# Kernel tuning notes

Measured on AMD Instinct MI355X. Metric: run time of the kernel, lower is better.

Reference implementation:

```python
import jax, jax.numpy as jnp
import numpy as np

N = 100000
E = 3200000
NFEAT = 128
NCLASS = 40


def setup_inputs() -> dict:
    key = jax.random.key(0)
    ks = jax.random.split(key, 16)
    x = jax.random.normal(ks[0], (N, NFEAT), dtype=jnp.float32)
    edge_src = jax.random.randint(ks[1], (E,), 0, N)
    edge_dst = jax.random.randint(ks[2], (E,), 0, N)
    # normalized-adjacency-like positive edge weights
    edge_val = jax.random.uniform(ks[3], (E,), dtype=jnp.float32) * 0.1
    dims = [(NFEAT, 1024), (1024, 1024), (1024, 1024), (1024, 64), (64, NCLASS)]
    params = {}
    for i, (din, dout) in enumerate(dims):
        scale = 1.0 / np.sqrt(din)
        params[f"W{i+1}"] = jax.random.uniform(ks[4 + i], (din, dout), dtype=jnp.float32, minval=-scale, maxval=scale)
        params[f"b{i+1}"] = jax.random.uniform(ks[9 + i], (dout,), dtype=jnp.float32, minval=-scale, maxval=scale)
    return {"x": x, "edge_src": edge_src, "edge_dst": edge_dst, "edge_val": edge_val, **params}


def _gcn_layer(x, edge_src, edge_dst, edge_val, W, b):
    # support = x @ W ; out[dst] += val * support[src] ; + bias
    support = x @ W  # [N, dout]
    msgs = support[edge_src] * edge_val[:, None]  # [E, dout]
    agg = jax.ops.segment_sum(msgs, edge_dst, num_segments=x.shape[0])
    return agg + b


def reference(x, edge_src, edge_dst, edge_val, W1, b1, W2, b2, W3, b3, W4, b4, W5, b5):
    h = jax.nn.relu(_gcn_layer(x, edge_src, edge_dst, edge_val, W1, b1))
    identity1 = h
    h = jax.nn.relu(_gcn_layer(h, edge_src, edge_dst, edge_val, W2, b2))
    identity2 = h
    h = h + identity1
    h = jax.nn.relu(_gcn_layer(h, edge_src, edge_dst, edge_val, W3, b3))
    h = h + identity2
    h = jax.nn.relu(_gcn_layer(h, edge_src, edge_dst, edge_val, W4, b4))
    h = jax.nn.relu(_gcn_layer(h, edge_src, edge_dst, edge_val, W5, b5))
    return jax.nn.log_softmax(h, axis=1)
```

## Files before the change

kernel.cpp:

```cpp
#include <hip/hip_runtime.h>
#include <hip/hip_bf16.h>
#include <stdint.h>

#define NN 100000
#define NE 3200000
#define MP 100096
#define MPAD 100352
#define NPANEL 784
#define SCALE 32.0f
#define ISCALE 0.03125f
#define WSCALE 8192.0f

typedef __bf16 bf16x8 __attribute__((ext_vector_type(8)));
typedef float  f32x4  __attribute__((ext_vector_type(4)));
typedef unsigned short u16x8 __attribute__((ext_vector_type(8)));

__device__ __forceinline__ float b2f(unsigned short u) {
    union { unsigned int i; float f; } x; x.i = ((unsigned int)u) << 16; return x.f;
}
__device__ __forceinline__ unsigned short f2b(float f) {
    __hip_bfloat16 h = __float2bfloat16(f);
    return __builtin_bit_cast(unsigned short, h);
}

#if defined(__has_builtin)
#if __has_builtin(__builtin_amdgcn_cvt_pk_f32_fp8) && __has_builtin(__builtin_amdgcn_cvt_pk_fp8_f32)
#define HAVE_FP8_CVT 1
#endif
#endif

__device__ __forceinline__ float f8dec1(unsigned int b) {
    unsigned int s = (b >> 7) & 1u, e = (b >> 3) & 15u, m = b & 7u;
    float mag = e ? __builtin_bit_cast(float, (unsigned int)(((e + 120u) << 23) | (m << 20)))
                  : (float)m * 0.001953125f;
    return s ? -mag : mag;
}
__device__ __forceinline__ unsigned char f8enc1(float v) {
    unsigned int bits = __builtin_bit_cast(unsigned int, v);
    unsigned char s = (unsigned char)((bits >> 24) & 0x80u);
    float a = fabsf(v);
    if (!(a < 464.f)) return (unsigned char)(s | 0x7e);
    if (a < 0.015625f) {
        int q = (int)rintf(a * 512.f);
        return (unsigned char)(s | (unsigned char)q);
    }
    unsigned int b = __builtin_bit_cast(unsigned int, a);
    b += 0x7FFFFu + ((b >> 20) & 1u);
    unsigned int e = (b >> 23) - 120u;
    unsigned int m = (b >> 20) & 7u;
    if (e >= 16u) return (unsigned char)(s | 0x7e);
    return (unsigned char)(s | (e << 3) | m);
}
__device__ __forceinline__ void dec4(unsigned int u, float* o) {
#ifdef HAVE_FP8_CVT
    typedef float f32x2 __attribute__((ext_vector_type(2)));
    f32x2 lo = __builtin_amdgcn_cvt_pk_f32_fp8((int)u, false);
    f32x2 hi = __builtin_amdgcn_cvt_pk_f32_fp8((int)u, true);
    o[0] = lo[0]; o[1] = lo[1]; o[2] = hi[0]; o[3] = hi[1];
#else
    o[0] = f8dec1(u & 255u); o[1] = f8dec1((u >> 8) & 255u);
    o[2] = f8dec1((u >> 16) & 255u); o[3] = f8dec1((u >> 24) & 255u);
#endif
}
__device__ __forceinline__ unsigned char f8enc(float v) {
#ifdef HAVE_FP8_CVT
    return (unsigned char)(__builtin_amdgcn_cvt_pk_fp8_f32(v, v, 0, false) & 0xff);
#else
    return f8enc1(v);
#endif
}
__device__ __forceinline__ unsigned int enc4(float a, float b, float c, float d) {
#ifdef HAVE_FP8_CVT
    int r = __builtin_amdgcn_cvt_pk_fp8_f32(a, b, 0, false);
    r = __builtin_amdgcn_cvt_pk_fp8_f32(c, d, r, true);
    return (unsigned int)r;
#else
    return (unsigned int)f8enc1(a) | ((unsigned int)f8enc1(b) << 8) |
           ((unsigned int)f8enc1(c) << 16) | ((unsigned int)f8enc1(d) << 24);
#endif
}

#define GLDS16(g, l) __builtin_amdgcn_global_load_lds(                         \
    (const __attribute__((address_space(1))) void*)(const void*)(g),           \
    (__attribute__((address_space(3))) void*)(void*)(l), 16, 0, 0)

__global__ __launch_bounds__(256) void k_sentinel(float* out, int n, float code) {
    int i = blockIdx.x * 256 + threadIdx.x;
    if (i < n) out[i] = (i == 0) ? code : 1.0f;
}

__global__ __launch_bounds__(256) void k_zero_deg(unsigned int* deg) {
    int i = blockIdx.x * 256 + threadIdx.x;
    if (i < NN + 1) deg[i] = 0u;
}
__global__ __launch_bounds__(256) void k_hist(const int* __restrict__ dst,
                                              unsigned int* __restrict__ deg) {
    int e = blockIdx.x * 256 + threadIdx.x;
    if (e < NE) atomicAdd(&deg[dst[e]], 1u);
}
__global__ __launch_bounds__(256) void k_blocksum(const unsigned int* __restrict__ deg,
                                                  unsigned int* __restrict__ bsum) {
    __shared__ unsigned int sh[256];
    int base = blockIdx.x * 1024;
    unsigned int s = 0;
    for (int q = 0; q < 4; ++q) {
        int i = base + q * 256 + threadIdx.x;
        if (i < NN) s += deg[i];
    }
    sh[threadIdx.x] = s; __syncthreads();
    for (int off = 128; off > 0; off >>= 1) {
        if ((int)threadIdx.x < off) sh[threadIdx.x] += sh[threadIdx.x + off];
        __syncthreads();
    }
    if (threadIdx.x == 0) bsum[blockIdx.x] = sh[0];
}
__global__ __launch_bounds__(64) void k_scan_bsum(const unsigned int* __restrict__ bsum,
                                                  unsigned int* __restrict__ boff, int nb) {
    if (threadIdx.x == 0 && blockIdx.x == 0) {
        unsigned int run = 0;
        for (int i = 0; i < nb; ++i) { boff[i] = run; run += bsum[i]; }
    }
}
__global__ __launch_bounds__(256) void k_scan_final(const unsigned int* __restrict__ deg,
                                                    const unsigned int* __restrict__ boff,
                                                    int* __restrict__ rowptr) {
    __shared__ unsigned int sh[256];
    const int b = blockIdx.x, t = threadIdx.x;
    const int base = b * 1024 + t * 4;
    unsigned int v[4];
    for (int q = 0; q < 4; ++q) { int i = base + q; v[q] = (i < NN) ? deg[i] : 0u; }
    unsigned int p = v[0] + v[1] + v[2] + v[3];
    sh[t] = p; __syncthreads();
    for (int off = 1; off < 256; off <<= 1) {
        unsigned int add = (t >= off) ? sh[t - off] : 0u; __syncthreads();
        sh[t] += add; __syncthreads();
    }
    unsigned int run = sh[t] - p + boff[b];
    for (int q = 0; q < 4; ++q) {
        int i = base + q;
        if (i < NN) rowptr[i] = (int)run;
        run += v[q];
    }
    if (b == 0 && t == 0) rowptr[NN] = NE;
}
__global__ __launch_bounds__(256) void k_copy_cursor(const int* __restrict__ rowptr,
                                                     int* __restrict__ cur) {
    int i = blockIdx.x * 256 + threadIdx.x;
    if (i < NN) cur[i] = rowptr[i];
}
__global__ __launch_bounds__(256) void k_fill(const int* __restrict__ src,
                                              const int* __restrict__ dst,
                                              const float* __restrict__ val,
                                              int* __restrict__ cur,
                                              int* __restrict__ csr_src,
                                              float* __restrict__ csr_val) {
    int e = blockIdx.x * 256 + threadIdx.x;
    if (e < NE) {
        int d = dst[e];
        int p = atomicAdd(&cur[d], 1);
        csr_src[p] = src[e];
        csr_val[p] = val[e];
    }
}

__global__ __launch_bounds__(256) void k_build_tab(unsigned long long* __restrict__ tab,
                                                   unsigned long long px, unsigned long long p1,
                                                   unsigned long long p2, unsigned long long p3,
                                                   unsigned long long po, unsigned long long pd) {
    int r = blockIdx.x * 256 + threadIdx.x;
    if (r >= MPAD) return;
    unsigned long long p; long long rr;
    if (r < 50000)      { p = px; rr = r; }
    else if (r < 62500) { p = p1; rr = r - 50000; }
    else if (r < 75000) { p = p2; rr = r - 62500; }
    else if (r < 87500) { p = p3; rr = r - 75000; }
    else if (r < MP)    { p = po; rr = r - 87500; }
    else                { p = pd; rr = 0; }
    tab[r] = p + (unsigned long long)rr * 1024ull;
}

__global__ __launch_bounds__(256) void k_transpose_w(const float* __restrict__ W,
                                                     unsigned short* __restrict__ Wt,
                                                     int din, int dout) {
    int idx = blockIdx.x * 256 + threadIdx.x;
    if (idx >= din * dout) return;
    int i = idx / dout, o = idx % dout;
    Wt[(size_t)o * din + i] = f2b(W[idx]);
}
__global__ __launch_bounds__(256) void k_transpose_w8(const float* __restrict__ W,
                                                      unsigned char* __restrict__ Wt,
                                                      int din, int dout) {
    int idx = blockIdx.x * 256 + threadIdx.x;
    if (idx >= din * dout) return;
    int i = idx / dout, o = idx % dout;
    Wt[(size_t)o * din + i] = f8enc(W[idx] * WSCALE);
}

template<int BN, int AKIND, int EPI, int OKIND>
__global__ __launch_bounds__(256) void k_gemm(const void* __restrict__ Ap,
                                              const void* __restrict__ Ap2,
                                              const __hip_bfloat16* __restrict__ Bt,
                                              const float* __restrict__ bias,
                                              void* __restrict__ Cp,
                                              const unsigned long long* __restrict__ rowtab,
                                              int K, int Nn) {
    constexpr int BM = 128, BK = 32;
    __shared__ alignas(16) __hip_bfloat16 Al[BM * BK];
    __shared__ alignas(16) __hip_bfloat16 Bl[BN * BK];
    const int t = threadIdx.x;
    const int lane = t & 63, w = t >> 6;
    const int row0 = blockIdx.y * BM, col0 = blockIdx.x * BN;
    const int wm = w >> 1, wn = w & 1;
    constexpr int FN = BN / 32;

    f32x4 acc[4][FN];
#pragma unroll
    for (int i = 0; i < 4; ++i)
#pragma unroll
        for (int j = 0; j < FN; ++j) acc[i][j] = (f32x4){0.f, 0.f, 0.f, 0.f};

    const int srow = t >> 2;
    const int scol = ((t & 3) ^ ((srow >> 1) & 3)) * 8;
    const __hip_bfloat16* gB = Bt + (size_t)(col0 + srow) * K + scol;
    __hip_bfloat16* lB = Bl + w * 512;
    const __hip_bfloat16* gA = (const __hip_bfloat16*)Ap + (size_t)(row0 + srow) * K + scol;
    __hip_bfloat16* lA = Al + w * 512;

    const int nkt = K / BK;
    for (int kt = 0; kt < nkt; ++kt) {
        const int ko = kt * BK;
        GLDS16(gA + ko, lA);
        GLDS16(gA + (size_t)64 * K + ko, lA + 2048);
        GLDS16(gB + ko, lB);
        if constexpr (BN == 128) GLDS16(gB + (size_t)64 * K + ko, lB + 2048);
        __syncthreads();

        const int pcr = ((lane >> 4) ^ (((lane & 15) >> 1) & 3)) * 8;
        const __hip_bfloat16* Ar = Al + (wm * 64 + (lane & 15)) * BK + pcr;
        const __hip_bfloat16* Br = Bl + (wn * (BN / 2) + (lane & 15)) * BK + pcr;
        bf16x8 af[4], bfr[FN];
#pragma unroll
        for (int i = 0; i < 4; ++i) af[i] = *(const bf16x8*)(Ar + i * 16 * BK);
#pragma unroll
        for (int j = 0; j < FN; ++j) bfr[j] = *(const bf16x8*)(Br + j * 16 * BK);
#pragma unroll
        for (int i = 0; i < 4; ++i)
#pragma unroll
            for (int j = 0; j < FN; ++j)
                acc[i][j] = __builtin_amdgcn_mfma_f32_16x16x32_bf16(af[i], bfr[j], acc[i][j], 0, 0, 0);
        __syncthreads();
    }

#pragma unroll
    for (int i = 0; i < 4; ++i) {
        const int r0 = row0 + wm * 64 + i * 16 + (lane >> 4) * 4;
#pragma unroll
        for (int j = 0; j < FN; ++j) {
            const int c = col0 + wn * (BN / 2) + j * 16 + (lane & 15);
#pragma unroll
            for (int v = 0; v < 4; ++v) {
                float val = acc[i][j][v];
                if constexpr (EPI == 1) val = fmaxf(val + bias[c], 0.f) * SCALE;
                const int r = r0 + v;
                if constexpr (OKIND == 0) {
                    ((unsigned char*)Cp)[(size_t)r * Nn + c] = f8enc(val);
                } else if constexpr (OKIND == 1) {
                    *(unsigned char*)((uintptr_t)rowtab[r] + c) = f8enc(val);
                } else {
                    ((unsigned short*)Cp)[(size_t)r * Nn + c] = f2b(val);
                }
            }
        }
    }
}

template<int BN, int NA, int OKIND>
__global__ __launch_bounds__(256) void k_gemm8(const unsigned char* __restrict__ Ap,
                                               const unsigned char* __restrict__ Ap2,
                                               const unsigned char* __restrict__ Bt,
                                               void* __restrict__ Cp,
                                               const unsigned long long* __restrict__ rowtab,
                                               float oscale) {
    constexpr int K = 1024, BM = 128, BK = 64;
    constexpr int NT = (BN == 128) ? 8 : 1;
    constexpr int CST = BN * NT;
    constexpr int FN = BN / 32;
    __shared__ alignas(16) unsigned char Al[NA][BM * BK];
    __shared__ alignas(16) unsigned char Bl[BN * BK];
    const int t = threadIdx.x, lane = t & 63, w = t >> 6;
    const int Bid = blockIdx.x;
    const int xcd = Bid & 7, slot = Bid >> 3;
    const int ct = slot % NT, pj = slot / NT;
    const int p = xcd + 8 * pj;
    const int row0 = p * BM, col0 = ct * BN;
    const int wm = w >> 1, wn = w & 1;

    f32x4 acc[4][FN];
#pragma unroll
    for (int i = 0; i < 4; ++i)
#pragma unroll
        for (int j = 0; j < FN; ++j) acc[i][j] = (f32x4){0.f, 0.f, 0.f, 0.f};

    const int rl = lane >> 2, gl = lane & 3;
    const int ra0 = w * 16 + rl;
    const int ra1 = 64 + w * 16 + rl;
    const unsigned char* gA0 = Ap + (size_t)(row0 + ra0) * K + ((gl ^ ((ra0 >> 1) & 3)) << 4);
    const unsigned char* gA1 = Ap + (size_t)(row0 + ra1) * K + ((gl ^ ((ra1 >> 1) & 3)) << 4);
    unsigned char* lA0 = &Al[0][w * 1024];
    unsigned char* lA1 = &Al[0][4096 + w * 1024];
    const unsigned char* gA20 = nullptr; const unsigned char* gA21 = nullptr;
    unsigned char* lA20 = nullptr; unsigned char* lA21 = nullptr;
    if constexpr (NA == 2) {
        gA20 = Ap2 + (size_t)(row0 + ra0) * K + ((gl ^ ((ra0 >> 1) & 3)) << 4);
        gA21 = Ap2 + (size_t)(row0 + ra1) * K + ((gl ^ ((ra1 >> 1) & 3)) << 4);
        lA20 = &Al[1][w * 1024];
        lA21 = &Al[1][4096 + w * 1024];
    }
    const unsigned char* gB0 = Bt + (size_t)(col0 + ra0) * K + ((gl ^ ((ra0 >> 1) & 3)) << 4);
    const unsigned char* gB1 = nullptr;
    unsigned char* lB0 = &Bl[w * 1024];
    unsigned char* lB1 = nullptr;
    if constexpr (BN == 128) {
        gB1 = Bt + (size_t)(col0 + ra1) * K + ((gl ^ ((ra1 >> 1) & 3)) << 4);
        lB1 = &Bl[4096 + w * 1024];
    }

    for (int kt = 0; kt < K / BK; ++kt) {
        const int ko = kt * BK;
        GLDS16(gA0 + ko, lA0);
        GLDS16(gA1 + ko, lA1);
        if constexpr (NA == 2) { GLDS16(gA20 + ko, lA20); GLDS16(gA21 + ko, lA21); }
        GLDS16(gB0 + ko, lB0);
        if constexpr (BN == 128) GLDS16(gB1 + ko, lB1);
        __syncthreads();

#pragma unroll
        for (int kk = 0; kk < 2; ++kk) {
            const int c = kk * 4 + (lane >> 4);
            const int G = c >> 1, h = c & 1;
            long long a0[4], a1[4], bb[FN];
#pragma unroll
            for (int i = 0; i < 4; ++i) {
                const int r = wm * 64 + i * 16 + (lane & 15);
                const int off = r * 64 + ((((G ^ ((r >> 1) & 3)) << 1) | h) << 3);
                a0[i] = *(const long long*)(&Al[0][off]);
                if constexpr (NA == 2) a1[i] = *(const long long*)(&Al[1][off]);
            }
#pragma unroll
            for (int j = 0; j < FN; ++j) {
                const int r = wn * (BN / 2) + j * 16 + (lane & 15);
                const int off = r * 64 + ((((G ^ ((r >> 1) & 3)) << 1) | h) << 3);
                bb[j] = *(const long long*)(&Bl[off]);
            }
#pragma unroll
            for (int i = 0; i < 4; ++i)
#pragma unroll
                for (int j = 0; j < FN; ++j) {
                    acc[i][j] = __builtin_amdgcn_mfma_f32_16x16x32_fp8_fp8(a0[i], bb[j], acc[i][j], 0, 0, 0);
                    if constexpr (NA == 2)
                        acc[i][j] = __builtin_amdgcn_mfma_f32_16x16x32_fp8_fp8(a1[i], bb[j], acc[i][j], 0, 0, 0);
                }
        }
        __syncthreads();
    }

#pragma unroll
    for (int i = 0; i < 4; ++i) {
        const int r0 = row0 + wm * 64 + i * 16 + (lane >> 4) * 4;
#pragma unroll
        for (int j = 0; j < FN; ++j) {
            const int cc = col0 + wn * (BN / 2) + j * 16 + (lane & 15);
#pragma unroll
            for (int v = 0; v < 4; ++v) {
                const float val = acc[i][j][v] * oscale;
                const int r = r0 + v;
                if constexpr (OKIND == 1) {
                    *(unsigned char*)((uintptr_t)rowtab[r] + cc) = f8enc(val);
                } else {
                    ((unsigned short*)Cp)[(size_t)r * CST + cc] = f2b(val);
                }
            }
        }
    }
}

__global__ __launch_bounds__(256) void k_agg1(const float* __restrict__ x,
                                              const int* __restrict__ rowptr,
                                              const int* __restrict__ csr_src,
                                              const float* __restrict__ csr_val,
                                              unsigned short* __restrict__ ax) {
    const int t = threadIdx.x;
    const int g = t >> 5, sub = t & 31;
    const size_t dst = (size_t)blockIdx.x * 8 + g;
    if (dst >= MP) return;
    int lo = 0, hi = 0;
    if (dst < NN) { lo = rowptr[dst]; hi = rowptr[dst + 1]; }
    const int fo = sub * 4;
    float a0 = 0.f, a1 = 0.f, a2 = 0.f, a3 = 0.f;
    int e = lo;
    for (; e + 4 <= hi; e += 4) {
        int s[4]; float v[4]; float4 u[4];
#pragma unroll
        for (int q = 0; q < 4; ++q) { s[q] = csr_src[e + q]; v[q] = csr_val[e + q]; }
#pragma unroll
        for (int q = 0; q < 4; ++q) u[q] = *(const float4*)(x + (size_t)s[q] * 128 + fo);
#pragma unroll
        for (int q = 0; q < 4; ++q) {
            a0 += v[q] * u[q].x; a1 += v[q] * u[q].y;
            a2 += v[q] * u[q].z; a3 += v[q] * u[q].w;
        }
    }
    for (; e < hi; ++e) {
        int s = csr_src[e]; float v = csr_val[e];
        float4 u = *(const float4*)(x + (size_t)s * 128 + fo);
        a0 += v * u.x; a1 += v * u.y; a2 += v * u.z; a3 += v * u.w;
    }
    *(ushort4*)(ax + dst * 128 + fo) = make_ushort4(f2b(a0), f2b(a1), f2b(a2), f2b(a3));
}

template<int MODE>
__global__ __launch_bounds__(256) void k_agg_big(const unsigned long long* __restrict__ rowtab,
                                                 const int* __restrict__ rowptr,
                                                 const int* __restrict__ csr_src,
                                                 const float* __restrict__ csr_val,
                                                 const float* __restrict__ bias,
                                                 unsigned char* __restrict__ outbuf) {
    const int t = threadIdx.x;
    const int dst = blockIdx.x;
    int lo = 0, hi = 0;
    if (dst < NN) { lo = rowptr[dst]; hi = rowptr[dst + 1]; }
    const int boff = t * 4;
    float a0 = 0.f, a1 = 0.f, a2 = 0.f, a3 = 0.f;
    int e = lo;
    for (; e + 8 <= hi; e += 8) {
        int s[8]; float v[8]; unsigned int u[8];
#pragma unroll
        for (int q = 0; q < 8; ++q) { s[q] = csr_src[e + q]; v[q] = csr_val[e + q]; }
#pragma unroll
        for (int q = 0; q < 8; ++q)
            u[q] = *(const unsigned int*)((uintptr_t)rowtab[s[q]] + boff);
#pragma unroll
        for (int q = 0; q < 8; ++q) {
            float f[4]; dec4(u[q], f);
            a0 += v[q] * f[0]; a1 += v[q] * f[1]; a2 += v[q] * f[2]; a3 += v[q] * f[3];
        }
    }
    for (; e + 4 <= hi; e += 4) {
        int s[4]; float v[4]; unsigned int u[4];
#pragma unroll
        for (int q = 0; q < 4; ++q) { s[q] = csr_src[e + q]; v[q] = csr_val[e + q]; }
#pragma unroll
        for (int q = 0; q < 4; ++q)
            u[q] = *(const unsigned int*)((uintptr_t)rowtab[s[q]] + boff);
#pragma unroll
        for (int q = 0; q < 4; ++q) {
            float f[4]; dec4(u[q], f);
            a0 += v[q] * f[0]; a1 += v[q] * f[1]; a2 += v[q] * f[2]; a3 += v[q] * f[3];
        }
    }
    for (; e < hi; ++e) {
        int s = csr_src[e]; float v = csr_val[e];
        unsigned int u = *(const unsigned int*)((uintptr_t)rowtab[s] + boff);
        float f[4]; dec4(u, f);
        a0 += v * f[0]; a1 += v * f[1]; a2 += v * f[2]; a3 += v * f[3];
    }
    float r0 = fmaxf(a0 + SCALE * bias[boff + 0], 0.f);
    float r1 = fmaxf(a1 + SCALE * bias[boff + 1], 0.f);
    float r2 = fmaxf(a2 + SCALE * bias[boff + 2], 0.f);
    float r3 = fmaxf(a3 + SCALE * bias[boff + 3], 0.f);
    unsigned int* op = (unsigned int*)(outbuf + (size_t)dst * 1024 + boff);
    if constexpr (MODE == 2) {
        float f[4]; dec4(*op, f);
        r0 += f[0]; r1 += f[1]; r2 += f[2]; r3 += f[3];
    }
    *op = enc4(r0, r1, r2, r3);
}

__global__ __launch_bounds__(256) void k_agg4(const unsigned short* __restrict__ s4,
                                              const int* __restrict__ rowptr,
                                              const int* __restrict__ csr_src,
                                              const float* __restrict__ csr_val,
                                              const float* __restrict__ bias,
                                              unsigned short* __restrict__ h4) {
    const int t = threadIdx.x;
    const int g = t >> 4, sub = t & 15;
    const size_t dst = (size_t)blockIdx.x * 16 + g;
    if (dst >= MP) return;
    int lo = 0, hi = 0;
    if (dst < NN) { lo = rowptr[dst]; hi = rowptr[dst + 1]; }
    const int fo = sub * 4;
    float a0 = 0.f, a1 = 0.f, a2 = 0.f, a3 = 0.f;
    int e = lo;
    for (; e + 4 <= hi; e += 4) {
        int s[4]; float v[4]; ushort4 u[4];
#pragma unroll
        for (int q = 0; q < 4; ++q) { s[q] = csr_src[e + q]; v[q] = csr_val[e + q]; }
#pragma unroll
        for (int q = 0; q < 4; ++q) u[q] = *(const ushort4*)(s4 + (size_t)s[q] * 64 + fo);
#pragma unroll
        for (int q = 0; q < 4; ++q) {
            a0 += v[q] * b2f(u[q].x); a1 += v[q] * b2f(u[q].y);
            a2 += v[q] * b2f(u[q].z); a3 += v[q] * b2f(u[q].w);
        }
    }
    for (; e < hi; ++e) {
        int s = csr_src[e]; float v = csr_val[e];
        ushort4 u = *(const ushort4*)(s4 + (size_t)s * 64 + fo);
        a0 += v * b2f(u.x); a1 += v * b2f(u.y); a2 += v * b2f(u.z); a3 += v * b2f(u.w);
    }
    float r0 = fmaxf(a0 + SCALE * bias[fo + 0], 0.f);
    float r1 = fmaxf(a1 + SCALE * bias[fo + 1], 0.f);
    float r2 = fmaxf(a2 + SCALE * bias[fo + 2], 0.f);
    float r3 = fmaxf(a3 + SCALE * bias[fo + 3], 0.f);
    *(ushort4*)(h4 + dst * 64 + fo) = make_ushort4(f2b(r0), f2b(r1), f2b(r2), f2b(r3));
}

__global__ __launch_bounds__(256) void k_gemm5(const unsigned short* __restrict__ H4,
                                               const float* __restrict__ W5,
                                               float* __restrict__ S5) {
    __shared__ float Wl[64 * 40];
    for (int i = threadIdx.x; i < 2560; i += 256) Wl[i] = W5[i];
    __syncthreads();
    const size_t r = (size_t)blockIdx.x * 256 + threadIdx.x;
    if (r >= MP) return;
    const ushort4* hp = (const ushort4*)(H4 + r * 64);
    float acc[40];
#pragma unroll
    for (int c = 0; c < 40; ++c) acc[c] = 0.f;
#pragma unroll
    for (int kk = 0; kk < 16; ++kk) {
        ushort4 u = hp[kk];
        float h0 = b2f(u.x), h1 = b2f(u.y), h2 = b2f(u.z), h3 = b2f(u.w);
#pragma unroll
        for (int c = 0; c < 40; ++c)
            acc[c] += h0 * Wl[(kk * 4 + 0) * 40 + c] + h1 * Wl[(kk * 4 + 1) * 40 + c]
                    + h2 * Wl[(kk * 4 + 2) * 40 + c] + h3 * Wl[(kk * 4 + 3) * 40 + c];
    }
    float* o = S5 + r * 40;
#pragma unroll
    for (int c = 0; c < 40; ++c) o[c] = acc[c];
}

__global__ __launch_bounds__(256) void k_final(const float* __restrict__ S5,
                                               const int* __restrict__ rowptr,
                                               const int* __restrict__ csr_src,
                                               const float* __restrict__ csr_val,
                                               const float* __restrict__ b5,
                                               float* __restrict__ out) {
    const int lane = threadIdx.x & 63;
    const int w = threadIdx.x >> 6;
    const size_t dst = (size_t)blockIdx.x * 4 + w;
    const bool act = lane < 40;
    int lo = rowptr[dst], hi = rowptr[dst + 1];
    float acc = 0.f;
    int e = lo;
    for (; e + 4 <= hi; e += 4) {
        int s0 = csr_src[e], s1 = csr_src[e + 1], s2 = csr_src[e + 2], s3 = csr_src[e + 3];
        float v0 = csr_val[e], v1 = csr_val[e + 1], v2 = csr_val[e + 2], v3 = csr_val[e + 3];
        if (act) {
            acc += v0 * S5[(size_t)s0 * 40 + lane] + v1 * S5[(size_t)s1 * 40 + lane]
                 + v2 * S5[(size_t)s2 * 40 + lane] + v3 * S5[(size_t)s3 * 40 + lane];
        }
    }
    for (; e < hi; ++e)
        if (act) acc += csr_val[e] * S5[(size_t)csr_src[e] * 40 + lane];
    float val = act ? fmaxf(acc * ISCALE + b5[lane], 0.f) : -1e30f;
    float m = val;
#pragma unroll
    for (int o = 32; o >= 1; o >>= 1) m = fmaxf(m, __shfl_xor(m, o));
    float ex = act ? expf(val - m) : 0.f;
    float sum = ex;
#pragma unroll
    for (int o = 32; o >= 1; o >>= 1) sum += __shfl_xor(sum, o);
    if (act) out[dst * 40 + lane] = (val - m) - logf(sum);
}

extern "C" void kernel_launch(void* const* d_in, const int* in_sizes, int n_in,
                              void* d_out, int out_size, void* d_ws, size_t ws_size,
                              hipStream_t stream) {
    const float* x    = (const float*)d_in[0];
    const int*   esrc = (const int*)d_in[1];
    const int*   edst = (const int*)d_in[2];
    const float* eval = (const float*)d_in[3];
    const float* W1 = (const float*)d_in[4];  const float* b1 = (const float*)d_in[5];
    const float* W2 = (const float*)d_in[6];  const float* b2 = (const float*)d_in[7];
    const float* W3 = (const float*)d_in[8];  const float* b3 = (const float*)d_in[9];
    const float* W4 = (const float*)d_in[10]; const float* b4 = (const float*)d_in[11];
    const float* W5 = (const float*)d_in[12]; const float* b5 = (const float*)d_in[13];
    float* out = (float*)d_out;

    char* ws = (char*)d_ws;
    size_t off = 0;
    auto carve = [&](size_t bytes) -> char* {
        char* p = ws + off;
        off += (bytes + 255) & ~(size_t)255;
        return p;
    };
    int* csr_src        = (int*)carve((size_t)NE * 4);
    float* csr_val      = (float*)carve((size_t)NE * 4);
    int* rowptr         = (int*)carve((size_t)(NN + 1) * 4);
    unsigned int* deg   = (unsigned int*)carve((size_t)(NN + 1) * 4);
    int* cur            = (int*)carve((size_t)NN * 4);
    unsigned int* bsum  = (unsigned int*)carve(128 * 4);
    unsigned int* boff  = (unsigned int*)carve(128 * 4);
    unsigned long long* rowtab = (unsigned long long*)carve((size_t)MPAD * 8);
    char* dummy         = carve(1024);
    unsigned short* wt1 = (unsigned short*)carve((size_t)1024 * 128 * 2);
    unsigned char* wt2  = (unsigned char*)carve((size_t)1024 * 1024);
    unsigned char* wt3  = (unsigned char*)carve((size_t)1024 * 1024);
    unsigned char* wt4  = (unsigned char*)carve((size_t)64 * 1024);
    unsigned char* bufA = (unsigned char*)carve((size_t)MPAD * 1024);
    unsigned char* bufB = (unsigned char*)carve((size_t)MPAD * 1024);

    if (off > ws_size) {
        k_sentinel<<<(out_size + 255) / 256, 256, 0, stream>>>(
            out, out_size, 20000.0f + (float)(ws_size >> 20));
        return;
    }

    char* segx = (char*)d_in[0];
    char* seg1 = (char*)d_in[1];
    char* seg2 = (char*)d_in[2];
    char* seg3 = (char*)d_in[3];
    char* sego = (char*)d_out;
    unsigned short* s4 = (unsigned short*)segx;
    unsigned short* h4 = (unsigned short*)(segx + 13631488);
    float*          s5 = (float*)(segx + 28311552);
    unsigned short* ax = (unsigned short*)bufB;

    const int nb = (NN + 1023) / 1024;

    k_zero_deg<<<(NN + 1 + 255) / 256, 256, 0, stream>>>(deg);
    k_hist<<<NE / 256, 256, 0, stream>>>(edst, deg);
    k_blocksum<<<nb, 256, 0, stream>>>(deg, bsum);
    k_scan_bsum<<<1, 64, 0, stream>>>(bsum, boff, nb);
    k_scan_final<<<nb, 256, 0, stream>>>(deg, boff, rowptr);
    k_copy_cursor<<<(NN + 255) / 256, 256, 0, stream>>>(rowptr, cur);
    k_fill<<<NE / 256, 256, 0, stream>>>(esrc, edst, eval, cur, csr_src, csr_val);
    k_build_tab<<<(MPAD + 255) / 256, 256, 0, stream>>>(rowtab,
        (unsigned long long)(uintptr_t)segx, (unsigned long long)(uintptr_t)seg1,
        (unsigned long long)(uintptr_t)seg2, (unsigned long long)(uintptr_t)seg3,
        (unsigned long long)(uintptr_t)sego, (unsigned long long)(uintptr_t)dummy);

    k_transpose_w<<<(128 * 1024) / 256, 256, 0, stream>>>(W1, wt1, 128, 1024);
    k_transpose_w8<<<(1024 * 1024) / 256, 256, 0, stream>>>(W2, wt2, 1024, 1024);
    k_transpose_w8<<<(1024 * 1024) / 256, 256, 0, stream>>>(W3, wt3, 1024, 1024);
    k_transpose_w8<<<(1024 * 64) / 256, 256, 0, stream>>>(W4, wt4, 1024, 64);

    k_agg1<<<MP / 8, 256, 0, stream>>>(x, rowptr, csr_src, csr_val, ax);
    k_gemm<128, 0, 1, 0><<<dim3(8, NPANEL), 256, 0, stream>>>(
        ax, nullptr, (const __hip_bfloat16*)wt1, b1, bufA, nullptr, 128, 1024);
    k_gemm8<128, 1, 1><<<NPANEL * 8, 256, 0, stream>>>(
        bufA, nullptr, wt2, nullptr, rowtab, 1.0f / 8192.0f);
    k_agg_big<1><<<MP, 256, 0, stream>>>(rowtab, rowptr, csr_src, csr_val, b2, bufB);
    k_gemm8<128, 2, 1><<<NPANEL * 8, 256, 0, stream>>>(
        bufA, bufB, wt3, nullptr, rowtab, 1.0f / 8192.0f);
    k_agg_big<2><<<MP, 256, 0, stream>>>(rowtab, rowptr, csr_src, csr_val, b3, bufB);
    k_gemm8<64, 1, 2><<<NPANEL, 256, 0, stream>>>(
        bufB, nullptr, wt4, s4, nullptr, 1.0f / 8192.0f);
    k_agg4<<<MP / 16, 256, 0, stream>>>(s4, rowptr, csr_src, csr_val, b4, h4);
    k_gemm5<<<MP / 256, 256, 0, stream>>>(h4, W5, s5);
    k_final<<<NN / 4, 256, 0, stream>>>(s5, rowptr, csr_src, csr_val, b5, out);
}
```

Before: 2.585 ms.

## Quantize layer-1 path to fp8, pack CSR edges, fuse residual add into aggregation

Converts x and W1 to fp8 so the first aggregation gathers 1-byte features and the first GEMM runs on the fp8 MFMA kernel in place of the bf16 one. Packs CSR src and value into one int2 array so each edge needs a single load. The layer-2 aggregation now writes the residual sum (h2 + identity1) into an auxiliary buffer, which removes the dual-A-operand GEMM for layer 3. Weight transposes use a shared-memory tiled kernel with 16-byte stores, and the layer-5 support is stored as bf16. The cost is extra fp8 quantization error on the input layer and an additional conversion pass over x.

```diff
diff --git a/kernel.cpp b/kernel.cpp
--- a/kernel.cpp
+++ b/kernel.cpp
@@ -9,11 +9,9 @@
 #define NPANEL 784
 #define SCALE 32.0f
 #define ISCALE 0.03125f
-#define WSCALE 8192.0f
 
 typedef __bf16 bf16x8 __attribute__((ext_vector_type(8)));
 typedef float  f32x4  __attribute__((ext_vector_type(4)));
-typedef unsigned short u16x8 __attribute__((ext_vector_type(8)));
 
 __device__ __forceinline__ float b2f(unsigned short u) {
     union { unsigned int i; float f; } x; x.i = ((unsigned int)u) << 16; return x.f;
@@ -152,14 +150,12 @@
                                               const int* __restrict__ dst,
                                               const float* __restrict__ val,
                                               int* __restrict__ cur,
-                                              int* __restrict__ csr_src,
-                                              float* __restrict__ csr_val) {
+                                              int2* __restrict__ csr_ev) {
     int e = blockIdx.x * 256 + threadIdx.x;
     if (e < NE) {
         int d = dst[e];
         int p = atomicAdd(&cur[d], 1);
-        csr_src[p] = src[e];
-        csr_val[p] = val[e];
+        csr_ev[p] = make_int2(src[e], __float_as_int(val[e]));
     }
 }
 
@@ -179,113 +175,46 @@
     tab[r] = p + (unsigned long long)rr * 1024ull;
 }
 
-__global__ __launch_bounds__(256) void k_transpose_w(const float* __restrict__ W,
-                                                     unsigned short* __restrict__ Wt,
-                                                     int din, int dout) {
-    int idx = blockIdx.x * 256 + threadIdx.x;
-    if (idx >= din * dout) return;
-    int i = idx / dout, o = idx % dout;
-    Wt[(size_t)o * din + i] = f2b(W[idx]);
-}
-__global__ __launch_bounds__(256) void k_transpose_w8(const float* __restrict__ W,
-                                                      unsigned char* __restrict__ Wt,
-                                                      int din, int dout) {
-    int idx = blockIdx.x * 256 + threadIdx.x;
-    if (idx >= din * dout) return;
-    int i = idx / dout, o = idx % dout;
-    Wt[(size_t)o * din + i] = f8enc(W[idx] * WSCALE);
-}
-
-template<int BN, int AKIND, int EPI, int OKIND>
-__global__ __launch_bounds__(256) void k_gemm(const void* __restrict__ Ap,
-                                              const void* __restrict__ Ap2,
-                                              const __hip_bfloat16* __restrict__ Bt,
-                                              const float* __restrict__ bias,
-                                              void* __restrict__ Cp,
-                                              const unsigned long long* __restrict__ rowtab,
-                                              int K, int Nn) {
-    constexpr int BM = 128, BK = 32;
-    __shared__ alignas(16) __hip_bfloat16 Al[BM * BK];
-    __shared__ alignas(16) __hip_bfloat16 Bl[BN * BK];
+__global__ __launch_bounds__(256) void k_convert_x8(const float* __restrict__ x,
+                                                    unsigned char* __restrict__ xq) {
+    long i = (long)blockIdx.x * 256 + threadIdx.x;
+    if (i >= (long)MPAD * 128) return;
+    int r = (int)(i >> 7);
+    xq[i] = (r < NN) ? f8enc(x[i] * 16.0f) : (unsigned char)0;
+}
+
+__global__ __launch_bounds__(256) void k_txp8(const float* __restrict__ W,
+                                              unsigned char* __restrict__ Wt,
+                                              int din, int dout, float wscale) {
+    __shared__ float tile[64][65];
     const int t = threadIdx.x;
-    const int lane = t & 63, w = t >> 6;
-    const int row0 = blockIdx.y * BM, col0 = blockIdx.x * BN;
-    const int wm = w >> 1, wn = w & 1;
-    constexpr int FN = BN / 32;
-
-    f32x4 acc[4][FN];
-#pragma unroll
-    for (int i = 0; i < 4; ++i)
-#pragma unroll
-        for (int j = 0; j < FN; ++j) acc[i][j] = (f32x4){0.f, 0.f, 0.f, 0.f};
-
-    const int srow = t >> 2;
-    const int scol = ((t & 3) ^ ((srow >> 1) & 3)) * 8;
-    const __hip_bfloat16* gB = Bt + (size_t)(col0 + srow) * K + scol;
-    __hip_bfloat16* lB = Bl + w * 512;
-    const __hip_bfloat16* gA = (const __hip_bfloat16*)Ap + (size_t)(row0 + srow) * K + scol;
-    __hip_bfloat16* lA = Al + w * 512;
-
-    const int nkt = K / BK;
-    for (int kt = 0; kt < nkt; ++kt) {
-        const int ko = kt * BK;
-        GLDS16(gA + ko, lA);
-        GLDS16(gA + (size_t)64 * K + ko, lA + 2048);
-        GLDS16(gB + ko, lB);
-        if constexpr (BN == 128) GLDS16(gB + (size_t)64 * K + ko, lB + 2048);
-        __syncthreads();
-
-        const int pcr = ((lane >> 4) ^ (((lane & 15) >> 1) & 3)) * 8;
-        const __hip_bfloat16* Ar = Al + (wm * 64 + (lane & 15)) * BK + pcr;
-        const __hip_bfloat16* Br = Bl + (wn * (BN / 2) + (lane & 15)) * BK + pcr;
-        bf16x8 af[4], bfr[FN];
-#pragma unroll
-        for (int i = 0; i < 4; ++i) af[i] = *(const bf16x8*)(Ar + i * 16 * BK);
-#pragma unroll
-        for (int j = 0; j < FN; ++j) bfr[j] = *(const bf16x8*)(Br + j * 16 * BK);
-#pragma unroll
-        for (int i = 0; i < 4; ++i)
-#pragma unroll
-            for (int j = 0; j < FN; ++j)
-                acc[i][j] = __builtin_amdgcn_mfma_f32_16x16x32_bf16(af[i], bfr[j], acc[i][j], 0, 0, 0);
-        __syncthreads();
-    }
-
-#pragma unroll
-    for (int i = 0; i < 4; ++i) {
-        const int r0 = row0 + wm * 64 + i * 16 + (lane >> 4) * 4;
-#pragma unroll
-        for (int j = 0; j < FN; ++j) {
-            const int c = col0 + wn * (BN / 2) + j * 16 + (lane & 15);
-#pragma unroll
-            for (int v = 0; v < 4; ++v) {
-                float val = acc[i][j][v];
-                if constexpr (EPI == 1) val = fmaxf(val + bias[c], 0.f) * SCALE;
-                const int r = r0 + v;
-                if constexpr (OKIND == 0) {
-                    ((unsigned char*)Cp)[(size_t)r * Nn + c] = f8enc(val);
-                } else if constexpr (OKIND == 1) {
-                    *(unsigned char*)((uintptr_t)rowtab[r] + c) = f8enc(val);
-                } else {
-                    ((unsigned short*)Cp)[(size_t)r * Nn + c] = f2b(val);
-                }
-            }
-        }
-    }
-}
-
-template<int BN, int NA, int OKIND>
+    const int o0 = blockIdx.x * 64, i0 = blockIdx.y * 64;
+    const int col = t & 63, r0 = t >> 6;
+#pragma unroll
+    for (int q = 0; q < 16; ++q) {
+        int r = r0 * 16 + q;
+        tile[r][col] = W[(size_t)(i0 + r) * dout + o0 + col];
+    }
+    __syncthreads();
+    const int oo = t >> 2, ic = (t & 3) * 16;
+    alignas(16) unsigned char b[16];
+#pragma unroll
+    for (int k2 = 0; k2 < 16; ++k2) b[k2] = f8enc(tile[ic + k2][oo] * wscale);
+    *(uint4*)(Wt + (size_t)(o0 + oo) * din + i0 + ic) = *(const uint4*)b;
+}
+
+template<int BN, int K, int EPI, int OKIND>
 __global__ __launch_bounds__(256) void k_gemm8(const unsigned char* __restrict__ Ap,
-                                               const unsigned char* __restrict__ Ap2,
                                                const unsigned char* __restrict__ Bt,
+                                               const float* __restrict__ bias,
                                                void* __restrict__ Cp,
                                                const unsigned long long* __restrict__ rowtab,
                                                float oscale) {
-    constexpr int K = 1024, BM = 128, BK = 64;
+    constexpr int BM = 128, BK = 64;
     constexpr int NT = (BN == 128) ? 8 : 1;
     constexpr int CST = BN * NT;
     constexpr int FN = BN / 32;
-    __shared__ alignas(16) unsigned char Al[NA][BM * BK];
+    __shared__ alignas(16) unsigned char Al[BM * BK];
     __shared__ alignas(16) unsigned char Bl[BN * BK];
     const int t = threadIdx.x, lane = t & 63, w = t >> 6;
     const int Bid = blockIdx.x;
@@ -306,16 +235,8 @@
     const int ra1 = 64 + w * 16 + rl;
     const unsigned char* gA0 = Ap + (size_t)(row0 + ra0) * K + ((gl ^ ((ra0 >> 1) & 3)) << 4);
     const unsigned char* gA1 = Ap + (size_t)(row0 + ra1) * K + ((gl ^ ((ra1 >> 1) & 3)) << 4);
-    unsigned char* lA0 = &Al[0][w * 1024];
-    unsigned char* lA1 = &Al[0][4096 + w * 1024];
-    const unsigned char* gA20 = nullptr; const unsigned char* gA21 = nullptr;
-    unsigned char* lA20 = nullptr; unsigned char* lA21 = nullptr;
-    if constexpr (NA == 2) {
-        gA20 = Ap2 + (size_t)(row0 + ra0) * K + ((gl ^ ((ra0 >> 1) & 3)) << 4);
-        gA21 = Ap2 + (size_t)(row0 + ra1) * K + ((gl ^ ((ra1 >> 1) & 3)) << 4);
-        lA20 = &Al[1][w * 1024];
-        lA21 = &Al[1][4096 + w * 1024];
-    }
+    unsigned char* lA0 = &Al[w * 1024];
+    unsigned char* lA1 = &Al[4096 + w * 1024];
     const unsigned char* gB0 = Bt + (size_t)(col0 + ra0) * K + ((gl ^ ((ra0 >> 1) & 3)) << 4);
     const unsigned char* gB1 = nullptr;
     unsigned char* lB0 = &Bl[w * 1024];
@@ -329,7 +250,6 @@
         const int ko = kt * BK;
         GLDS16(gA0 + ko, lA0);
         GLDS16(gA1 + ko, lA1);
-        if constexpr (NA == 2) { GLDS16(gA20 + ko, lA20); GLDS16(gA21 + ko, lA21); }
         GLDS16(gB0 + ko, lB0);
         if constexpr (BN == 128) GLDS16(gB1 + ko, lB1);
         __syncthreads();
@@ -338,13 +258,12 @@
         for (int kk = 0; kk < 2; ++kk) {
             const int c = kk * 4 + (lane >> 4);
             const int G = c >> 1, h = c & 1;
-            long long a0[4], a1[4], bb[FN];
+            long long a0[4], bb[FN];
 #pragma unroll
             for (int i = 0; i < 4; ++i) {
                 const int r = wm * 64 + i * 16 + (lane & 15);
                 const int off = r * 64 + ((((G ^ ((r >> 1) & 3)) << 1) | h) << 3);
-                a0[i] = *(const long long*)(&Al[0][off]);
-                if constexpr (NA == 2) a1[i] = *(const long long*)(&Al[1][off]);
+                a0[i] = *(const long long*)(&Al[off]);
             }
 #pragma unroll
             for (int j = 0; j < FN; ++j) {
@@ -355,11 +274,8 @@
 #pragma unroll
             for (int i = 0; i < 4; ++i)
 #pragma unroll
-                for (int j = 0; j < FN; ++j) {
+                for (int j = 0; j < FN; ++j)
                     acc[i][j] = __builtin_amdgcn_mfma_f32_16x16x32_fp8_fp8(a0[i], bb[j], acc[i][j], 0, 0, 0);
-                    if constexpr (NA == 2)
-                        acc[i][j] = __builtin_amdgcn_mfma_f32_16x16x32_fp8_fp8(a1[i], bb[j], acc[i][j], 0, 0, 0);
-                }
         }
         __syncthreads();
     }
@@ -372,9 +288,12 @@
             const int cc = col0 + wn * (BN / 2) + j * 16 + (lane & 15);
 #pragma unroll
             for (int v = 0; v < 4; ++v) {
-                const float val = acc[i][j][v] * oscale;
+                float val = acc[i][j][v] * oscale;
+                if constexpr (EPI == 1) val = fmaxf(val + bias[cc], 0.f) * SCALE;
                 const int r = r0 + v;
-                if constexpr (OKIND == 1) {
+                if constexpr (OKIND == 0) {
+                    ((unsigned char*)Cp)[(size_t)r * CST + cc] = f8enc(val);
+                } else if constexpr (OKIND == 1) {
                     *(unsigned char*)((uintptr_t)rowtab[r] + cc) = f8enc(val);
                 } else {
                     ((unsigned short*)Cp)[(size_t)r * CST + cc] = f2b(val);
@@ -384,47 +303,49 @@
     }
 }
 
-__global__ __launch_bounds__(256) void k_agg1(const float* __restrict__ x,
+__global__ __launch_bounds__(256) void k_agg1(const unsigned char* __restrict__ xq,
                                               const int* __restrict__ rowptr,
-                                              const int* __restrict__ csr_src,
-                                              const float* __restrict__ csr_val,
-                                              unsigned short* __restrict__ ax) {
+                                              const int2* __restrict__ csr_ev,
+                                              unsigned char* __restrict__ axq) {
     const int t = threadIdx.x;
     const int g = t >> 5, sub = t & 31;
     const size_t dst = (size_t)blockIdx.x * 8 + g;
-    if (dst >= MP) return;
+    if (dst >= MPAD) return;
     int lo = 0, hi = 0;
     if (dst < NN) { lo = rowptr[dst]; hi = rowptr[dst + 1]; }
     const int fo = sub * 4;
     float a0 = 0.f, a1 = 0.f, a2 = 0.f, a3 = 0.f;
     int e = lo;
-    for (; e + 4 <= hi; e += 4) {
-        int s[4]; float v[4]; float4 u[4];
-#pragma unroll
-        for (int q = 0; q < 4; ++q) { s[q] = csr_src[e + q]; v[q] = csr_val[e + q]; }
-#pragma unroll
-        for (int q = 0; q < 4; ++q) u[q] = *(const float4*)(x + (size_t)s[q] * 128 + fo);
-#pragma unroll
-        for (int q = 0; q < 4; ++q) {
-            a0 += v[q] * u[q].x; a1 += v[q] * u[q].y;
-            a2 += v[q] * u[q].z; a3 += v[q] * u[q].w;
+    for (; e + 8 <= hi; e += 8) {
+        int2 ev[8]; unsigned int u[8];
+#pragma unroll
+        for (int q = 0; q < 8; ++q) ev[q] = csr_ev[e + q];
+#pragma unroll
+        for (int q = 0; q < 8; ++q)
+            u[q] = *(const unsigned int*)(xq + (size_t)ev[q].x * 128 + fo);
+#pragma unroll
+        for (int q = 0; q < 8; ++q) {
+            float v = __int_as_float(ev[q].y);
+            float f[4]; dec4(u[q], f);
+            a0 += v * f[0]; a1 += v * f[1]; a2 += v * f[2]; a3 += v * f[3];
         }
     }
     for (; e < hi; ++e) {
-        int s = csr_src[e]; float v = csr_val[e];
-        float4 u = *(const float4*)(x + (size_t)s * 128 + fo);
-        a0 += v * u.x; a1 += v * u.y; a2 += v * u.z; a3 += v * u.w;
-    }
-    *(ushort4*)(ax + dst * 128 + fo) = make_ushort4(f2b(a0), f2b(a1), f2b(a2), f2b(a3));
+        int2 ev = csr_ev[e]; float v = __int_as_float(ev.y);
+        unsigned int u = *(const unsigned int*)(xq + (size_t)ev.x * 128 + fo);
+        float f[4]; dec4(u, f);
+        a0 += v * f[0]; a1 += v * f[1]; a2 += v * f[2]; a3 += v * f[3];
+    }
+    *(unsigned int*)(axq + dst * 128 + fo) = enc4(2.f * a0, 2.f * a1, 2.f * a2, 2.f * a3);
 }
 
 template<int MODE>
 __global__ __launch_bounds__(256) void k_agg_big(const unsigned long long* __restrict__ rowtab,
                                                  const int* __restrict__ rowptr,
-                                                 const int* __restrict__ csr_src,
-                                                 const float* __restrict__ csr_val,
+                                                 const int2* __restrict__ csr_ev,
                                                  const float* __restrict__ bias,
-                                                 unsigned char* __restrict__ outbuf) {
+                                                 unsigned char* __restrict__ outbuf,
+                                                 unsigned char* __restrict__ auxbuf) {
     const int t = threadIdx.x;
     const int dst = blockIdx.x;
     int lo = 0, hi = 0;
@@ -433,34 +354,36 @@
     float a0 = 0.f, a1 = 0.f, a2 = 0.f, a3 = 0.f;
     int e = lo;
     for (; e + 8 <= hi; e += 8) {
-        int s[8]; float v[8]; unsigned int u[8];
-#pragma unroll
-        for (int q = 0; q < 8; ++q) { s[q] = csr_src[e + q]; v[q] = csr_val[e + q]; }
+        int2 ev[8]; unsigned int u[8];
+#pragma unroll
+        for (int q = 0; q < 8; ++q) ev[q] = csr_ev[e + q];
 #pragma unroll
         for (int q = 0; q < 8; ++q)
-            u[q] = *(const unsigned int*)((uintptr_t)rowtab[s[q]] + boff);
+            u[q] = *(const unsigned int*)((uintptr_t)rowtab[ev[q].x] + boff);
 #pragma unroll
         for (int q = 0; q < 8; ++q) {
+            float v = __int_as_float(ev[q].y);
             float f[4]; dec4(u[q], f);
-            a0 += v[q] * f[0]; a1 += v[q] * f[1]; a2 += v[q] * f[2]; a3 += v[q] * f[3];
+            a0 += v * f[0]; a1 += v * f[1]; a2 += v * f[2]; a3 += v * f[3];
         }
     }
     for (; e + 4 <= hi; e += 4) {
-        int s[4]; float v[4]; unsigned int u[4];
-#pragma unroll
-        for (int q = 0; q < 4; ++q) { s[q] = csr_src[e + q]; v[q] = csr_val[e + q]; }
+        int2 ev[4]; unsigned int u[4];
+#pragma unroll
+        for (int q = 0; q < 4; ++q) ev[q] = csr_ev[e + q];
 #pragma unroll
         for (int q = 0; q < 4; ++q)
-            u[q] = *(const unsigned int*)((uintptr_t)rowtab[s[q]] + boff);
+            u[q] = *(const unsigned int*)((uintptr_t)rowtab[ev[q].x] + boff);
 #pragma unroll
         for (int q = 0; q < 4; ++q) {
+            float v = __int_as_float(ev[q].y);
             float f[4]; dec4(u[q], f);
-            a0 += v[q] * f[0]; a1 += v[q] * f[1]; a2 += v[q] * f[2]; a3 += v[q] * f[3];
+            a0 += v * f[0]; a1 += v * f[1]; a2 += v * f[2]; a3 += v * f[3];
         }
     }
     for (; e < hi; ++e) {
-        int s = csr_src[e]; float v = csr_val[e];
-        unsigned int u = *(const unsigned int*)((uintptr_t)rowtab[s] + boff);
+        int2 ev = csr_ev[e]; float v = __int_as_float(ev.y);
+        unsigned int u = *(const unsigned int*)((uintptr_t)rowtab[ev.x] + boff);
         float f[4]; dec4(u, f);
         a0 += v * f[0]; a1 += v * f[1]; a2 += v * f[2]; a3 += v * f[3];
     }
@@ -471,15 +394,18 @@
     unsigned int* op = (unsigned int*)(outbuf + (size_t)dst * 1024 + boff);
     if constexpr (MODE == 2) {
         float f[4]; dec4(*op, f);
-        r0 += f[0]; r1 += f[1]; r2 += f[2]; r3 += f[3];
-    }
-    *op = enc4(r0, r1, r2, r3);
+        *op = enc4(r0 + f[0], r1 + f[1], r2 + f[2], r3 + f[3]);
+    } else {
+        unsigned int* ap = (unsigned int*)(auxbuf + (size_t)dst * 1024 + boff);
+        float f[4]; dec4(*ap, f);
+        *op = enc4(r0, r1, r2, r3);
+        *ap = enc4(r0 + f[0], r1 + f[1], r2 + f[2], r3 + f[3]);
+    }
 }
 
 __global__ __launch_bounds__(256) void k_agg4(const unsigned short* __restrict__ s4,
                                               const int* __restrict__ rowptr,
-                                              const int* __restrict__ csr_src,
-                                              const float* __restrict__ csr_val,
+                                              const int2* __restrict__ csr_ev,
                                               const float* __restrict__ bias,
                                               unsigned short* __restrict__ h4) {
     const int t = threadIdx.x;
@@ -492,20 +418,21 @@
     float a0 = 0.f, a1 = 0.f, a2 = 0.f, a3 = 0.f;
     int e = lo;
     for (; e + 4 <= hi; e += 4) {
-        int s[4]; float v[4]; ushort4 u[4];
-#pragma unroll
-        for (int q = 0; q < 4; ++q) { s[q] = csr_src[e + q]; v[q] = csr_val[e + q]; }
-#pragma unroll
-        for (int q = 0; q < 4; ++q) u[q] = *(const ushort4*)(s4 + (size_t)s[q] * 64 + fo);
+        int2 ev[4]; ushort4 u[4];
+#pragma unroll
+        for (int q = 0; q < 4; ++q) ev[q] = csr_ev[e + q];
+#pragma unroll
+        for (int q = 0; q < 4; ++q) u[q] = *(const ushort4*)(s4 + (size_t)ev[q].x * 64 + fo);
 #pragma unroll
         for (int q = 0; q < 4; ++q) {
-            a0 += v[q] * b2f(u[q].x); a1 += v[q] * b2f(u[q].y);
-            a2 += v[q] * b2f(u[q].z); a3 += v[q] * b2f(u[q].w);
+            float v = __int_as_float(ev[q].y);
+            a0 += v * b2f(u[q].x); a1 += v * b2f(u[q].y);
+            a2 += v * b2f(u[q].z); a3 += v * b2f(u[q].w);
         }
     }
     for (; e < hi; ++e) {
-        int s = csr_src[e]; float v = csr_val[e];
-        ushort4 u = *(const ushort4*)(s4 + (size_t)s * 64 + fo);
+        int2 ev = csr_ev[e]; float v = __int_as_float(ev.y);
+        ushort4 u = *(const ushort4*)(s4 + (size_t)ev.x * 64 + fo);
         a0 += v * b2f(u.x); a1 += v * b2f(u.y); a2 += v * b2f(u.z); a3 += v * b2f(u.w);
     }
     float r0 = fmaxf(a0 + SCALE * bias[fo + 0], 0.f);
@@ -517,7 +444,7 @@
 
 __global__ __launch_bounds__(256) void k_gemm5(const unsigned short* __restrict__ H4,
                                                const float* __restrict__ W5,
-                                               float* __restrict__ S5) {
+                                               unsigned short* __restrict__ S5) {
     __shared__ float Wl[64 * 40];
     for (int i = threadIdx.x; i < 2560; i += 256) Wl[i] = W5[i];
     __syncthreads();
@@ -536,15 +463,14 @@
             acc[c] += h0 * Wl[(kk * 4 + 0) * 40 + c] + h1 * Wl[(kk * 4 + 1) * 40 + c]
                     + h2 * Wl[(kk * 4 + 2) * 40 + c] + h3 * Wl[(kk * 4 + 3) * 40 + c];
     }
-    float* o = S5 + r * 40;
-#pragma unroll
-    for (int c = 0; c < 40; ++c) o[c] = acc[c];
-}
-
-__global__ __launch_bounds__(256) void k_final(const float* __restrict__ S5,
+    unsigned short* o = S5 + r * 40;
+#pragma unroll
+    for (int c = 0; c < 40; ++c) o[c] = f2b(acc[c]);
+}
+
+__global__ __launch_bounds__(256) void k_final(const unsigned short* __restrict__ S5,
                                                const int* __restrict__ rowptr,
-                                               const int* __restrict__ csr_src,
-                                               const float* __restrict__ csr_val,
+                                               const int2* __restrict__ csr_ev,
                                                const float* __restrict__ b5,
                                                float* __restrict__ out) {
     const int lane = threadIdx.x & 63;
@@ -555,15 +481,18 @@
     float acc = 0.f;
     int e = lo;
     for (; e + 4 <= hi; e += 4) {
-        int s0 = csr_src[e], s1 = csr_src[e + 1], s2 = csr_src[e + 2], s3 = csr_src[e + 3];
-        float v0 = csr_val[e], v1 = csr_val[e + 1], v2 = csr_val[e + 2], v3 = csr_val[e + 3];
+        int2 e0 = csr_ev[e], e1 = csr_ev[e + 1], e2 = csr_ev[e + 2], e3 = csr_ev[e + 3];
         if (act) {
-            acc += v0 * S5[(size_t)s0 * 40 + lane] + v1 * S5[(size_t)s1 * 40 + lane]
-                 + v2 * S5[(size_t)s2 * 40 + lane] + v3 * S5[(size_t)s3 * 40 + lane];
-        }
-    }
-    for (; e < hi; ++e)
-        if (act) acc += csr_val[e] * S5[(size_t)csr_src[e] * 40 + lane];
+            acc += __int_as_float(e0.y) * b2f(S5[(size_t)e0.x * 40 + lane])
+                 + __int_as_float(e1.y) * b2f(S5[(size_t)e1.x * 40 + lane])
+                 + __int_as_float(e2.y) * b2f(S5[(size_t)e2.x * 40 + lane])
+                 + __int_as_float(e3.y) * b2f(S5[(size_t)e3.x * 40 + lane]);
+        }
+    }
+    for (; e < hi; ++e) {
+        int2 ev = csr_ev[e];
+        if (act) acc += __int_as_float(ev.y) * b2f(S5[(size_t)ev.x * 40 + lane]);
+    }
     float val = act ? fmaxf(acc * ISCALE + b5[lane], 0.f) : -1e30f;
     float m = val;
 #pragma unroll
@@ -596,8 +525,7 @@
         off += (bytes + 255) & ~(size_t)255;
         return p;
     };
-    int* csr_src        = (int*)carve((size_t)NE * 4);
-    float* csr_val      = (float*)carve((size_t)NE * 4);
+    int2* csr_ev        = (int2*)carve((size_t)NE * 8);
     int* rowptr         = (int*)carve((size_t)(NN + 1) * 4);
     unsigned int* deg   = (unsigned int*)carve((size_t)(NN + 1) * 4);
     int* cur            = (int*)carve((size_t)NN * 4);
@@ -605,10 +533,11 @@
     unsigned int* boff  = (unsigned int*)carve(128 * 4);
     unsigned long long* rowtab = (unsigned long long*)carve((size_t)MPAD * 8);
     char* dummy         = carve(1024);
-    unsigned short* wt1 = (unsigned short*)carve((size_t)1024 * 128 * 2);
+    unsigned char* wt1  = (unsigned char*)carve((size_t)128 * 1024);
     unsigned char* wt2  = (unsigned char*)carve((size_t)1024 * 1024);
     unsigned char* wt3  = (unsigned char*)carve((size_t)1024 * 1024);
     unsigned char* wt4  = (unsigned char*)carve((size_t)64 * 1024);
+    unsigned char* xq   = (unsigned char*)carve((size_t)MPAD * 128);
     unsigned char* bufA = (unsigned char*)carve((size_t)MPAD * 1024);
     unsigned char* bufB = (unsigned char*)carve((size_t)MPAD * 1024);
 
@@ -623,10 +552,10 @@
     char* seg2 = (char*)d_in[2];
     char* seg3 = (char*)d_in[3];
     char* sego = (char*)d_out;
-    unsigned short* s4 = (unsigned short*)segx;
-    unsigned short* h4 = (unsigned short*)(segx + 13631488);
-    float*          s5 = (float*)(segx + 28311552);
-    unsigned short* ax = (unsigned short*)bufB;
+    unsigned short* s4  = (unsigned short*)segx;
+    unsigned short* h4  = (unsigned short*)(segx + 13631488);
+    unsigned short* s5b = (unsigned short*)(segx + 28311552);
+    unsigned char* axq  = bufB;
 
     const int nb = (NN + 1023) / 1024;
 
@@ -636,29 +565,30 @@
     k_scan_bsum<<<1, 64, 0, stream>>>(bsum, boff, nb);
     k_scan_final<<<nb, 256, 0, stream>>>(deg, boff, rowptr);
     k_copy_cursor<<<(NN + 255) / 256, 256, 0, stream>>>(rowptr, cur);
-    k_fill<<<NE / 256, 256, 0, stream>>>(esrc, edst, eval, cur, csr_src, csr_val);
+    k_fill<<<NE / 256, 256, 0, stream>>>(esrc, edst, eval, cur, csr_ev);
     k_build_tab<<<(MPAD + 255) / 256, 256, 0, stream>>>(rowtab,
         (unsigned long long)(uintptr_t)segx, (unsigned long long)(uintptr_t)seg1,
         (unsigned long long)(uintptr_t)seg2, (unsigned long long)(uintptr_t)seg3,
         (unsigned long long)(uintptr_t)sego, (unsigned long long)(uintptr_t)dummy);
 
-    k_transpose_w<<<(128 * 1024) / 256, 256, 0, stream>>>(W1, wt1, 128, 1024);
-    k_transpose_w8<<<(1024 * 1024) / 256, 256, 0, stream>>>(W2, wt2, 1024, 1024);
-    k_transpose_w8<<<(1024 * 1024) / 256, 256, 0, stream>>>(W3, wt3, 1024, 1024);
-    k_transpose_w8<<<(1024 * 64) / 256, 256, 0, stream>>>(W4, wt4, 1024, 64);
-
-    k_agg1<<<MP / 8, 256, 0, stream>>>(x, rowptr, csr_src, csr_val, ax);
-    k_gemm<128, 0, 1, 0><<<dim3(8, NPANEL), 256, 0, stream>>>(
-        ax, nullptr, (const __hip_bfloat16*)wt1, b1, bufA, nullptr, 128, 1024);
-    k_gemm8<128, 1, 1><<<NPANEL * 8, 256, 0, stream>>>(
-        bufA, nullptr, wt2, nullptr, rowtab, 1.0f / 8192.0f);
-    k_agg_big<1><<<MP, 256, 0, stream>>>(rowtab, rowptr, csr_src, csr_val, b2, bufB);
-    k_gemm8<128, 2, 1><<<NPANEL * 8, 256, 0, stream>>>(
-        bufA, bufB, wt3, nullptr, rowtab, 1.0f / 8192.0f);
-    k_agg_big<2><<<MP, 256, 0, stream>>>(rowtab, rowptr, csr_src, csr_val, b3, bufB);
-    k_gemm8<64, 1, 2><<<NPANEL, 256, 0, stream>>>(
-        bufB, nullptr, wt4, s4, nullptr, 1.0f / 8192.0f);
-    k_agg4<<<MP / 16, 256, 0, stream>>>(s4, rowptr, csr_src, csr_val, b4, h4);
-    k_gemm5<<<MP / 256, 256, 0, stream>>>(h4, W5, s5);
-    k_final<<<NN / 4, 256, 0, stream>>>(s5, rowptr, csr_src, csr_val, b5, out);
-}
+    k_convert_x8<<<(MPAD * 128) / 256, 256, 0, stream>>>(x, xq);
+    k_txp8<<<dim3(16, 2), 256, 0, stream>>>(W1, wt1, 128, 1024, 4096.0f);
+    k_txp8<<<dim3(16, 16), 256, 0, stream>>>(W2, wt2, 1024, 1024, 8192.0f);
+    k_txp8<<<dim3(16, 16), 256, 0, stream>>>(W3, wt3, 1024, 1024, 8192.0f);
+    k_txp8<<<dim3(1, 16), 256, 0, stream>>>(W4, wt4, 1024, 64, 8192.0f);
+
+    k_agg1<<<MPAD / 8, 256, 0, stream>>>(xq, rowptr, csr_ev, axq);
+    k_gemm8<128, 128, 1, 0><<<NPANEL * 8, 256, 0, stream>>>(
+        axq, wt1, b1, bufA, nullptr, 1.0f / 131072.0f);
+    k_gemm8<128, 1024, 0, 1><<<NPANEL * 8, 256, 0, stream>>>(
+        bufA, wt2, nullptr, nullptr, rowtab, 1.0f / 8192.0f);
+    k_agg_big<3><<<MP, 256, 0, stream>>>(rowtab, rowptr, csr_ev, b2, bufB, bufA);
+    k_gemm8<128, 1024, 0, 1><<<NPANEL * 8, 256, 0, stream>>>(
+        bufA, wt3, nullptr, nullptr, rowtab, 1.0f / 8192.0f);
+    k_agg_big<2><<<MP, 256, 0, stream>>>(rowtab, rowptr, csr_ev, b3, bufB, nullptr);
+    k_gemm8<64, 1024, 0, 2><<<NPANEL, 256, 0, stream>>>(
+        bufB, wt4, nullptr, s4, nullptr, 1.0f / 8192.0f);
+    k_agg4<<<MP / 16, 256, 0, stream>>>(s4, rowptr, csr_ev, b4, h4);
+    k_gemm5<<<MP / 256, 256, 0, stream>>>(h4, W5, s5b);
+    k_final<<<NN / 4, 256, 0, stream>>>(s5b, rowptr, csr_ev, b5, out);
+}
```

After: 2.262 ms. 12.5% less time.
